# Optimization experiments

Measured on AMD Instinct MI355X. Metric: run time of the kernel, lower is better.

The kernel has to match this reference:

```python
import jax, jax.numpy as jnp
import numpy as np

B, T, D_MODEL, D_HEAD = 8, 2048, 1024, 64


def setup_inputs() -> dict:
    key = jax.random.key(0)
    kx, kk, kq, kv = jax.random.split(key, 4)
    x = jax.random.normal(kx, (B, T, D_MODEL), dtype=jnp.float32)
    # causal (tril) eos mask: 1 where attention allowed, 0 where masked
    tril = jnp.tril(jnp.ones((T, T), dtype=jnp.int32))
    eos_mask = jnp.broadcast_to(tril, (B, T, T))
    scale = 1.0 / np.sqrt(D_MODEL)
    Wk = jax.random.normal(kk, (D_MODEL, D_HEAD), dtype=jnp.float32) * scale
    Wq = jax.random.normal(kq, (D_MODEL, D_HEAD), dtype=jnp.float32) * scale
    Wv = jax.random.normal(kv, (D_MODEL, D_HEAD), dtype=jnp.float32) * scale
    return {"x": x, "eos_mask": eos_mask, "Wk": Wk, "Wq": Wq, "Wv": Wv}


def reference(x, eos_mask, Wk, Wq, Wv):
    # x: [B,T,C]; Wk/Wq/Wv: [C,Dh] (equivalent to nn.Linear(d_model, d_head, bias=False))
    Bx, Tx, C = x.shape
    k = jnp.einsum('btc,cd->btd', x, Wk)  # [B,T,Dh]
    q = jnp.einsum('btc,cd->btd', x, Wq)  # [B,T,Dh]
    v = jnp.einsum('btc,cd->btd', x, Wv)  # [B,T,Dh]
    # NOTE: original scales by 1/sqrt(C) = 1/sqrt(d_model), not 1/sqrt(d_head)
    wei = jnp.einsum('btd,bsd->bts', q, k) / jnp.sqrt(jnp.float32(C))  # [B,T,T]
    wei = jnp.where(eos_mask[:Bx, :Tx, :Tx] == 0, -jnp.inf, wei)
    wei = jax.nn.softmax(wei, axis=-1)
    # dropout p=0.0 (identity)
    out = jnp.einsum('bts,bsd->btd', wei, v)  # [B,T,Dh]
    return out
```

## Files before the change

### kernel.cpp

```cpp
#include <hip/hip_runtime.h>
#include <hip/hip_bf16.h>

typedef short bf16x8 __attribute__((ext_vector_type(8)));
typedef float f32x4 __attribute__((ext_vector_type(4)));
typedef unsigned short u16;
typedef u16 u16x8 __attribute__((ext_vector_type(8)));

constexpr int TT = 2048, CC = 1024, DH = 64, NB = 8;
constexpr float SCALE = 0.03125f;
constexpr int OUT_N4  = NB * TT * DH / 4;
constexpr int LSUM_N4 = NB * TT / 4;

__device__ __forceinline__ u16 f2b(float f) {
    __hip_bfloat16 h = __float2bfloat16(f);
    return *reinterpret_cast<u16*>(&h);
}
__device__ __forceinline__ float b2f(u16 b) {
    __hip_bfloat16 h = *reinterpret_cast<__hip_bfloat16*>(&b);
    return __bfloat162float(h);
}

__global__ __launch_bounds__(256)
void wconv_kernel(const float* __restrict__ Wk, const float* __restrict__ Wq,
                  const float* __restrict__ Wv, u16* __restrict__ wtB)
{
    int idx = blockIdx.x * 256 + threadIdx.x;
    int c = idx >> 7;
    int k8 = idx & 127;
    int m = c >> 6, d = c & 63;
    const float* wp = (m == 0) ? Wk : (m == 1) ? Wq : Wv;
    u16x8 o;
    #pragma unroll
    for (int j = 0; j < 8; ++j) o[j] = f2b(wp[(size_t)(k8 * 8 + j) * DH + d]);
    *reinterpret_cast<u16x8*>(&wtB[(size_t)c * CC + k8 * 8]) = o;
}

__global__ __launch_bounds__(256)
void zero_kernel(float4* __restrict__ outv, float4* __restrict__ lsumv)
{
    int i = blockIdx.x * 256 + threadIdx.x;
    float4 z = {0.f, 0.f, 0.f, 0.f};
    if (i < OUT_N4) outv[i] = z;
    else            lsumv[i - OUT_N4] = z;
}

__global__ __launch_bounds__(128)
void qkv_proj_kernel(const float* __restrict__ x, const u16* __restrict__ wtB,
                     u16* __restrict__ kB, u16* __restrict__ qB,
                     u16* __restrict__ vTB)
{
    __shared__ __align__(16) u16 xb[32 * 40];
    __shared__ __align__(16) u16 wt[96 * 40];

    const int tid = threadIdx.x;
    const int l = tid & 63, w = tid >> 6;
    const int lan15 = l & 15, lq = l >> 4;
    const int row0 = blockIdx.x * 32;
    const int ny = blockIdx.y;

    f32x4 acc[6];
    #pragma unroll
    for (int nt = 0; nt < 6; ++nt) acc[nt] = {0.f, 0.f, 0.f, 0.f};

    const int srow = tid >> 2, sk8 = tid & 3;

    for (int kc = 0; kc < CC; kc += 32) {
        __syncthreads();
        {
            const float* xp = &x[(size_t)(row0 + srow) * CC + kc + sk8 * 8];
            float4 a = *(const float4*)xp;
            float4 bq = *(const float4*)(xp + 4);
            u16x8 o;
            o[0]=f2b(a.x); o[1]=f2b(a.y); o[2]=f2b(a.z); o[3]=f2b(a.w);
            o[4]=f2b(bq.x); o[5]=f2b(bq.y); o[6]=f2b(bq.z); o[7]=f2b(bq.w);
            *reinterpret_cast<u16x8*>(&xb[srow * 40 + sk8 * 8]) = o;
        }
        #pragma unroll
        for (int i = 0; i < 3; ++i) {
            int idx = tid + 128 * i;
            int crow = idx >> 2, ck8 = idx & 3;
            *reinterpret_cast<u16x8*>(&wt[crow * 40 + ck8 * 8]) =
                *reinterpret_cast<const u16x8*>(
                    &wtB[(size_t)(ny * 96 + crow) * CC + kc + ck8 * 8]);
        }
        __syncthreads();

        bf16x8 af = *reinterpret_cast<const bf16x8*>(&xb[(16 * w + lan15) * 40 + lq * 8]);
        #pragma unroll
        for (int nt = 0; nt < 6; ++nt) {
            bf16x8 bfr = *reinterpret_cast<const bf16x8*>(&wt[(16 * nt + lan15) * 40 + lq * 8]);
            acc[nt] = __builtin_amdgcn_mfma_f32_16x16x32_bf16(af, bfr, acc[nt], 0, 0, 0);
        }
    }

    #pragma unroll
    for (int nt = 0; nt < 6; ++nt)
        #pragma unroll
        for (int r = 0; r < 4; ++r) {
            int cg = ny * 96 + nt * 16 + lan15;
            int m = cg >> 6, d = cg & 63;
            int rowg = row0 + 16 * w + lq * 4 + r;
            float val = acc[nt][r];
            if (m == 1) val *= SCALE;
            u16 bv = f2b(val);
            if (m == 0)      kB[(size_t)rowg * DH + d] = bv;
            else if (m == 1) qB[(size_t)rowg * DH + d] = bv;
            else vTB[(size_t)((rowg >> 11) * DH + d) * TT + (rowg & 2047)] = bv;
        }
}

__global__ __launch_bounds__(256)
void attn_kernel(const u16* __restrict__ qB, const u16* __restrict__ kB,
                 const u16* __restrict__ vTB, float* __restrict__ out,
                 float* __restrict__ lsumBuf)
{
    __shared__ __align__(16) u16 Kb[64 * 72];
    __shared__ __align__(16) u16 Vt[64 * 72];
    __shared__ __align__(16) u16 Pw[4 * 16 * 72];

    const int tid = threadIdx.x;
    const int l = tid & 63, w = tid >> 6;
    const int lan15 = l & 15, lq = l >> 4;
    const int b = blockIdx.y, bx = blockIdx.x;

    int qx = 0, ci = 0;
    #pragma unroll
    for (int m = 0; m < 8; ++m) {
        int gs = 2 * m * (m + 1), sz = 4 * (m + 1);
        if (bx >= gs && bx < gs + sz) {
            int o = bx - gs;
            int rr = o / (m + 1);
            ci = o - rr * (m + 1);
            qx = 4 * m + rr;
        }
    }
    const int q0 = qx * 64;
    const size_t rowB = (size_t)b * TT;

    bf16x8 qf0, qf1;
    {
        const u16* qp = &qB[(rowB + q0 + 16 * w + lan15) * DH + lq * 8];
        qf0 = *reinterpret_cast<const bf16x8*>(qp);
        qf1 = *reinterpret_cast<const bf16x8*>(qp + 32);
    }

    f32x4 acc_o[4];
    #pragma unroll
    for (int nt = 0; nt < 4; ++nt) acc_o[nt] = {0.f, 0.f, 0.f, 0.f};
    float lsum[4] = {0.f, 0.f, 0.f, 0.f};

    u16* psh = &Pw[w * 16 * 72];
    const int t1 = min(ci * 4 + 4, qx + 1);

    for (int t = ci * 4; t < t1; ++t) {
        __syncthreads();
        #pragma unroll
        for (int i = 0; i < 2; ++i) {
            int g = tid + 256 * i;
            int r = g >> 3, c8 = (g & 7) * 8;
            *reinterpret_cast<u16x8*>(&Kb[r * 72 + c8]) =
                *reinterpret_cast<const u16x8*>(&kB[(rowB + t * 64 + r) * DH + c8]);
            *reinterpret_cast<u16x8*>(&Vt[r * 72 + c8]) =
                *reinterpret_cast<const u16x8*>(&vTB[((size_t)b * DH + r) * TT + t * 64 + c8]);
        }
        __syncthreads();

        const bool diag = (t == qx);
        #pragma unroll
        for (int nt = 0; nt < 4; ++nt) {
            f32x4 s = {0.f, 0.f, 0.f, 0.f};
            bf16x8 k0 = *reinterpret_cast<const bf16x8*>(&Kb[(nt * 16 + lan15) * 72 + lq * 8]);
            bf16x8 k1 = *reinterpret_cast<const bf16x8*>(&Kb[(nt * 16 + lan15) * 72 + 32 + lq * 8]);
            s = __builtin_amdgcn_mfma_f32_16x16x32_bf16(qf0, k0, s, 0, 0, 0);
            s = __builtin_amdgcn_mfma_f32_16x16x32_bf16(qf1, k1, s, 0, 0, 0);
            #pragma unroll
            for (int r = 0; r < 4; ++r) {
                int rq = q0 + 16 * w + lq * 4 + r;
                int jc = t * 64 + nt * 16 + lan15;
                float p = 0.f;
                if (!diag || jc <= rq) p = __expf(s[r]);
                u16 pb = f2b(p);
                lsum[r] += b2f(pb);
                psh[(lq * 4 + r) * 72 + nt * 16 + lan15] = pb;
            }
        }
        bf16x8 pf0 = *reinterpret_cast<const bf16x8*>(&psh[lan15 * 72 + lq * 8]);
        bf16x8 pf1 = *reinterpret_cast<const bf16x8*>(&psh[lan15 * 72 + 32 + lq * 8]);
        #pragma unroll
        for (int nt = 0; nt < 4; ++nt) {
            bf16x8 v0 = *reinterpret_cast<const bf16x8*>(&Vt[(nt * 16 + lan15) * 72 + lq * 8]);
            bf16x8 v1 = *reinterpret_cast<const bf16x8*>(&Vt[(nt * 16 + lan15) * 72 + 32 + lq * 8]);
            acc_o[nt] = __builtin_amdgcn_mfma_f32_16x16x32_bf16(pf0, v0, acc_o[nt], 0, 0, 0);
            acc_o[nt] = __builtin_amdgcn_mfma_f32_16x16x32_bf16(pf1, v1, acc_o[nt], 0, 0, 0);
        }
    }

    #pragma unroll
    for (int r = 0; r < 4; ++r) {
        float tsum = lsum[r];
        tsum += __shfl_xor(tsum, 1);
        tsum += __shfl_xor(tsum, 2);
        tsum += __shfl_xor(tsum, 4);
        tsum += __shfl_xor(tsum, 8);
        lsum[r] = tsum;
    }
    if (lan15 == 0) {
        #pragma unroll
        for (int r = 0; r < 4; ++r)
            atomicAdd(&lsumBuf[rowB + q0 + 16 * w + lq * 4 + r], lsum[r]);
    }
    #pragma unroll
    for (int nt = 0; nt < 4; ++nt)
        #pragma unroll
        for (int r = 0; r < 4; ++r) {
            int rq = q0 + 16 * w + lq * 4 + r;
            atomicAdd(&out[(rowB + rq) * DH + nt * 16 + lan15], acc_o[nt][r]);
        }
}

__global__ __launch_bounds__(256)
void finalize_kernel(float4* __restrict__ outv, const float* __restrict__ lsumBuf)
{
    int i = blockIdx.x * 256 + threadIdx.x;
    float4 o = outv[i];
    float inv = 1.0f / lsumBuf[i >> 4];
    o.x *= inv; o.y *= inv; o.z *= inv; o.w *= inv;
    outv[i] = o;
}

extern "C" void kernel_launch(void* const* d_in, const int* in_sizes, int n_in,
                              void* d_out, int out_size, void* d_ws, size_t ws_size,
                              hipStream_t stream) {
    const float* x  = (const float*)d_in[0];
    const float* Wk = (const float*)d_in[2];
    const float* Wq = (const float*)d_in[3];
    const float* Wv = (const float*)d_in[4];

    char* ws = (char*)d_ws;
    u16* wtB     = (u16*)(ws);
    u16* qB      = (u16*)(ws + 393216);
    u16* kB      = (u16*)(ws + 393216 + 2097152);
    u16* vTB     = (u16*)(ws + 393216 + 2 * 2097152);
    float* lsumBuf = (float*)(ws + 393216 + 3 * 2097152);
    float* out = (float*)d_out;

    wconv_kernel<<<dim3(96), dim3(256), 0, stream>>>(Wk, Wq, Wv, wtB);
    zero_kernel<<<dim3(OUT_N4 / 256 + LSUM_N4 / 256), dim3(256), 0, stream>>>(
        (float4*)out, (float4*)lsumBuf);
    qkv_proj_kernel<<<dim3(512, 2), dim3(128), 0, stream>>>(x, wtB, kB, qB, vTB);
    attn_kernel<<<dim3(144, NB), dim3(256), 0, stream>>>(qB, kB, vTB, out, lsumBuf);
    finalize_kernel<<<dim3(OUT_N4 / 256), dim3(256), 0, stream>>>((float4*)out, lsumBuf);
}
```

Measured before the change: 268.6 us.

## Replace atomic accumulation with per-chunk partial slabs and restructure QKV projection

The attention kernel now writes per-key-chunk partial outputs and row sums into separate slabs instead of atomically adding into a zeroed output, and the finalize kernel reduces the slabs and normalizes. This drops the zero kernel and the float atomics. The QKV projection now runs one 256-thread block per 32 rows covering all 192 output columns with a 64-wide K step, so x is read and converted once instead of twice. V is stored row-major and transposed into shared memory inside attention, and the row sum now accumulates fp32 probabilities rather than bf16-rounded ones. The costs are extra workspace traffic for the slabs and scattered LDS stores for the transpose.

```diff
diff --git a/kernel.cpp b/kernel.cpp
--- a/kernel.cpp
+++ b/kernel.cpp
@@ -8,16 +8,11 @@
 
 constexpr int TT = 2048, CC = 1024, DH = 64, NB = 8;
 constexpr float SCALE = 0.03125f;
-constexpr int OUT_N4  = NB * TT * DH / 4;
-constexpr int LSUM_N4 = NB * TT / 4;
+constexpr int OUT_N4 = NB * TT * DH / 4;
 
 __device__ __forceinline__ u16 f2b(float f) {
     __hip_bfloat16 h = __float2bfloat16(f);
     return *reinterpret_cast<u16*>(&h);
-}
-__device__ __forceinline__ float b2f(u16 b) {
-    __hip_bfloat16 h = *reinterpret_cast<__hip_bfloat16*>(&b);
-    return __bfloat162float(h);
 }
 
 __global__ __launch_bounds__(256)
@@ -36,60 +31,56 @@
 }
 
 __global__ __launch_bounds__(256)
-void zero_kernel(float4* __restrict__ outv, float4* __restrict__ lsumv)
-{
-    int i = blockIdx.x * 256 + threadIdx.x;
-    float4 z = {0.f, 0.f, 0.f, 0.f};
-    if (i < OUT_N4) outv[i] = z;
-    else            lsumv[i - OUT_N4] = z;
-}
-
-__global__ __launch_bounds__(128)
 void qkv_proj_kernel(const float* __restrict__ x, const u16* __restrict__ wtB,
                      u16* __restrict__ kB, u16* __restrict__ qB,
-                     u16* __restrict__ vTB)
-{
-    __shared__ __align__(16) u16 xb[32 * 40];
-    __shared__ __align__(16) u16 wt[96 * 40];
+                     u16* __restrict__ vB)
+{
+    __shared__ __align__(16) u16 xb[32 * 72];
+    __shared__ __align__(16) u16 wt[192 * 72];
 
     const int tid = threadIdx.x;
     const int l = tid & 63, w = tid >> 6;
     const int lan15 = l & 15, lq = l >> 4;
     const int row0 = blockIdx.x * 32;
-    const int ny = blockIdx.y;
+    const int wr = 16 * (w & 1);
+    const int wc = (w >> 1) * 96;
 
     f32x4 acc[6];
     #pragma unroll
     for (int nt = 0; nt < 6; ++nt) acc[nt] = {0.f, 0.f, 0.f, 0.f};
 
-    const int srow = tid >> 2, sk8 = tid & 3;
-
-    for (int kc = 0; kc < CC; kc += 32) {
+    const int xr = tid >> 3, xk8 = (tid & 7) * 8;
+
+    for (int kc = 0; kc < CC; kc += 64) {
         __syncthreads();
         {
-            const float* xp = &x[(size_t)(row0 + srow) * CC + kc + sk8 * 8];
+            const float* xp = &x[(size_t)(row0 + xr) * CC + kc + xk8];
             float4 a = *(const float4*)xp;
             float4 bq = *(const float4*)(xp + 4);
             u16x8 o;
             o[0]=f2b(a.x); o[1]=f2b(a.y); o[2]=f2b(a.z); o[3]=f2b(a.w);
             o[4]=f2b(bq.x); o[5]=f2b(bq.y); o[6]=f2b(bq.z); o[7]=f2b(bq.w);
-            *reinterpret_cast<u16x8*>(&xb[srow * 40 + sk8 * 8]) = o;
-        }
-        #pragma unroll
-        for (int i = 0; i < 3; ++i) {
-            int idx = tid + 128 * i;
-            int crow = idx >> 2, ck8 = idx & 3;
-            *reinterpret_cast<u16x8*>(&wt[crow * 40 + ck8 * 8]) =
-                *reinterpret_cast<const u16x8*>(
-                    &wtB[(size_t)(ny * 96 + crow) * CC + kc + ck8 * 8]);
-        }
-        __syncthreads();
-
-        bf16x8 af = *reinterpret_cast<const bf16x8*>(&xb[(16 * w + lan15) * 40 + lq * 8]);
-        #pragma unroll
-        for (int nt = 0; nt < 6; ++nt) {
-            bf16x8 bfr = *reinterpret_cast<const bf16x8*>(&wt[(16 * nt + lan15) * 40 + lq * 8]);
-            acc[nt] = __builtin_amdgcn_mfma_f32_16x16x32_bf16(af, bfr, acc[nt], 0, 0, 0);
+            *reinterpret_cast<u16x8*>(&xb[xr * 72 + xk8]) = o;
+        }
+        #pragma unroll
+        for (int i = 0; i < 6; ++i) {
+            int idx = tid + 256 * i;
+            int crow = idx >> 3, ck8 = (idx & 7) * 8;
+            *reinterpret_cast<u16x8*>(&wt[crow * 72 + ck8]) =
+                *reinterpret_cast<const u16x8*>(&wtB[(size_t)crow * CC + kc + ck8]);
+        }
+        __syncthreads();
+
+        #pragma unroll
+        for (int ks = 0; ks < 2; ++ks) {
+            bf16x8 af = *reinterpret_cast<const bf16x8*>(
+                &xb[(wr + lan15) * 72 + ks * 32 + lq * 8]);
+            #pragma unroll
+            for (int nt = 0; nt < 6; ++nt) {
+                bf16x8 bfr = *reinterpret_cast<const bf16x8*>(
+                    &wt[(wc + nt * 16 + lan15) * 72 + ks * 32 + lq * 8]);
+                acc[nt] = __builtin_amdgcn_mfma_f32_16x16x32_bf16(af, bfr, acc[nt], 0, 0, 0);
+            }
         }
     }
 
@@ -97,22 +88,21 @@
     for (int nt = 0; nt < 6; ++nt)
         #pragma unroll
         for (int r = 0; r < 4; ++r) {
-            int cg = ny * 96 + nt * 16 + lan15;
+            int cg = wc + nt * 16 + lan15;
             int m = cg >> 6, d = cg & 63;
-            int rowg = row0 + 16 * w + lq * 4 + r;
+            int rowg = row0 + wr + lq * 4 + r;
             float val = acc[nt][r];
             if (m == 1) val *= SCALE;
             u16 bv = f2b(val);
-            if (m == 0)      kB[(size_t)rowg * DH + d] = bv;
-            else if (m == 1) qB[(size_t)rowg * DH + d] = bv;
-            else vTB[(size_t)((rowg >> 11) * DH + d) * TT + (rowg & 2047)] = bv;
+            u16* dst = (m == 0) ? kB : (m == 1) ? qB : vB;
+            dst[(size_t)rowg * DH + d] = bv;
         }
 }
 
 __global__ __launch_bounds__(256)
 void attn_kernel(const u16* __restrict__ qB, const u16* __restrict__ kB,
-                 const u16* __restrict__ vTB, float* __restrict__ out,
-                 float* __restrict__ lsumBuf)
+                 const u16* __restrict__ vB, float* __restrict__ outPart,
+                 float* __restrict__ lsumPart)
 {
     __shared__ __align__(16) u16 Kb[64 * 72];
     __shared__ __align__(16) u16 Vt[64 * 72];
@@ -160,8 +150,10 @@
             int r = g >> 3, c8 = (g & 7) * 8;
             *reinterpret_cast<u16x8*>(&Kb[r * 72 + c8]) =
                 *reinterpret_cast<const u16x8*>(&kB[(rowB + t * 64 + r) * DH + c8]);
-            *reinterpret_cast<u16x8*>(&Vt[r * 72 + c8]) =
-                *reinterpret_cast<const u16x8*>(&vTB[((size_t)b * DH + r) * TT + t * 64 + c8]);
+            u16x8 vv = *reinterpret_cast<const u16x8*>(&vB[(rowB + t * 64 + r) * DH + c8]);
+            #pragma unroll
+            for (int j = 0; j < 8; ++j)
+                Vt[(c8 + j) * 72 + r] = vv[j];
         }
         __syncthreads();
 
@@ -175,13 +167,14 @@
             s = __builtin_amdgcn_mfma_f32_16x16x32_bf16(qf1, k1, s, 0, 0, 0);
             #pragma unroll
             for (int r = 0; r < 4; ++r) {
-                int rq = q0 + 16 * w + lq * 4 + r;
-                int jc = t * 64 + nt * 16 + lan15;
-                float p = 0.f;
-                if (!diag || jc <= rq) p = __expf(s[r]);
-                u16 pb = f2b(p);
-                lsum[r] += b2f(pb);
-                psh[(lq * 4 + r) * 72 + nt * 16 + lan15] = pb;
+                float p = __expf(s[r]);
+                if (diag) {
+                    int rq = q0 + 16 * w + lq * 4 + r;
+                    int jc = t * 64 + nt * 16 + lan15;
+                    if (jc > rq) p = 0.f;
+                }
+                lsum[r] += p;
+                psh[(lq * 4 + r) * 72 + nt * 16 + lan15] = f2b(p);
             }
         }
         bf16x8 pf0 = *reinterpret_cast<const bf16x8*>(&psh[lan15 * 72 + lq * 8]);
@@ -204,28 +197,41 @@
         tsum += __shfl_xor(tsum, 8);
         lsum[r] = tsum;
     }
+    const size_t slab = (size_t)(ci * NB + b);
     if (lan15 == 0) {
         #pragma unroll
         for (int r = 0; r < 4; ++r)
-            atomicAdd(&lsumBuf[rowB + q0 + 16 * w + lq * 4 + r], lsum[r]);
+            lsumPart[slab * TT + q0 + 16 * w + lq * 4 + r] = lsum[r];
     }
     #pragma unroll
     for (int nt = 0; nt < 4; ++nt)
         #pragma unroll
         for (int r = 0; r < 4; ++r) {
             int rq = q0 + 16 * w + lq * 4 + r;
-            atomicAdd(&out[(rowB + rq) * DH + nt * 16 + lan15], acc_o[nt][r]);
-        }
-}
-
-__global__ __launch_bounds__(256)
-void finalize_kernel(float4* __restrict__ outv, const float* __restrict__ lsumBuf)
+            outPart[(slab * TT + rq) * DH + nt * 16 + lan15] = acc_o[nt][r];
+        }
+}
+
+__global__ __launch_bounds__(256)
+void finalize_kernel(float4* __restrict__ outv, const float4* __restrict__ outPart,
+                     const float* __restrict__ lsumPart)
 {
     int i = blockIdx.x * 256 + threadIdx.x;
-    float4 o = outv[i];
-    float inv = 1.0f / lsumBuf[i >> 4];
-    o.x *= inv; o.y *= inv; o.z *= inv; o.w *= inv;
-    outv[i] = o;
+    int br = i >> 4;
+    int row = br & (TT - 1);
+    int b = br >> 11;
+    int nc = (row >> 8) + 1;
+    float4 s = {0.f, 0.f, 0.f, 0.f};
+    float ls = 0.f;
+    for (int ci = 0; ci < nc; ++ci) {
+        size_t slab = (size_t)(ci * NB + b);
+        float4 p = outPart[slab * (TT * DH / 4) + (i & (TT * DH / 4 - 1))];
+        s.x += p.x; s.y += p.y; s.z += p.z; s.w += p.w;
+        ls += lsumPart[slab * TT + row];
+    }
+    float inv = 1.0f / ls;
+    s.x *= inv; s.y *= inv; s.z *= inv; s.w *= inv;
+    outv[i] = s;
 }
 
 extern "C" void kernel_launch(void* const* d_in, const int* in_sizes, int n_in,
@@ -237,17 +243,17 @@
     const float* Wv = (const float*)d_in[4];
 
     char* ws = (char*)d_ws;
-    u16* wtB     = (u16*)(ws);
-    u16* qB      = (u16*)(ws + 393216);
-    u16* kB      = (u16*)(ws + 393216 + 2097152);
-    u16* vTB     = (u16*)(ws + 393216 + 2 * 2097152);
-    float* lsumBuf = (float*)(ws + 393216 + 3 * 2097152);
+    u16* wtB = (u16*)(ws);
+    u16* qB  = (u16*)(ws + (1 << 20));
+    u16* kB  = (u16*)(ws + 3 * (1 << 20));
+    u16* vB  = (u16*)(ws + 5 * (1 << 20));
+    float* outPart  = (float*)(ws + 8 * (1 << 20));
+    float* lsumPart = (float*)(ws + 40 * (1 << 20));
     float* out = (float*)d_out;
 
     wconv_kernel<<<dim3(96), dim3(256), 0, stream>>>(Wk, Wq, Wv, wtB);
-    zero_kernel<<<dim3(OUT_N4 / 256 + LSUM_N4 / 256), dim3(256), 0, stream>>>(
-        (float4*)out, (float4*)lsumBuf);
-    qkv_proj_kernel<<<dim3(512, 2), dim3(128), 0, stream>>>(x, wtB, kB, qB, vTB);
-    attn_kernel<<<dim3(144, NB), dim3(256), 0, stream>>>(qB, kB, vTB, out, lsumBuf);
-    finalize_kernel<<<dim3(OUT_N4 / 256), dim3(256), 0, stream>>>((float4*)out, lsumBuf);
-}
+    qkv_proj_kernel<<<dim3(512), dim3(256), 0, stream>>>(x, wtB, kB, qB, vB);
+    attn_kernel<<<dim3(144, NB), dim3(256), 0, stream>>>(qB, kB, vB, outPart, lsumPart);
+    finalize_kernel<<<dim3(OUT_N4 / 256), dim3(256), 0, stream>>>(
+        (float4*)out, (const float4*)outPart, lsumPart);
+}
```

Result: no change. 268.0 us (-0.2%).
